# Optimization experiments

Measured on AMD Instinct MI355X. Metric: run time of the kernel, lower is better.

The kernel has to match this reference:

```python
import jax, jax.numpy as jnp
import numpy as np

EPS = 1e-12
H = 256
W = 256
RANK = 4
CTX = 1024
BATCH = 32
FF = (H + W) * RANK * 4  # 8192
STD = 0.001


def _norm(x, axis):
    # torch: (x - mean) / sqrt(var(unbiased) + eps)
    m = jnp.mean(x, axis=axis, keepdims=True)
    v = jnp.var(x, axis=axis, keepdims=True, ddof=1)
    return (x - m) / jnp.sqrt(v + EPS)


def _norm_polar(x):
    # x: [B, N, 2]; magnitude-normalize relative to per-batch max magnitude
    x_abs = jnp.sqrt(x[..., 0] ** 2 + x[..., 1] ** 2 + EPS)          # [B, N]
    h = x_abs / (jnp.max(x_abs, axis=-1, keepdims=True) + EPS)       # [B, N]
    xn = x / (x_abs[..., None] + EPS)                                # [B, N, 2]
    return jnp.stack([h * xn[..., 0], h * xn[..., 1]], axis=-1)


def setup_inputs() -> dict:
    key = jax.random.key(0)
    ks = jax.random.split(key, 12)

    def lin(k, fan_in, shape):
        b = 1.0 / np.sqrt(fan_in)
        return jax.random.uniform(k, shape, jnp.float32, -b, b)

    weights_static = jnp.concatenate([
        jax.random.normal(ks[9], (1, H, W, 2), jnp.float32) * STD,
        jax.random.normal(ks[10], (1, H, W, 2), jnp.float32) * STD
        + jnp.array([1.0, 0.0], jnp.float32),
    ], axis=0)  # [2, H, W, 2]

    return {
        "x": jax.random.normal(ks[0], (BATCH, CTX), jnp.float32),
        "W_in": lin(ks[1], CTX, (FF, CTX)),
        "b_in": lin(ks[2], CTX, (FF,)),
        "W_gate": lin(ks[3], CTX, (FF, CTX)),
        "b_gate": lin(ks[4], CTX, (FF,)),
        "W_t": lin(ks[5], FF, (FF, FF)),
        "b_t": lin(ks[6], FF, (FF,)),
        "conv_w": lin(ks[7], RANK, (RANK, RANK)),  # 1x1 conv kernel [out, in]
        "conv_b": lin(ks[8], RANK, (RANK,)),
        "weights_static": weights_static,
        "weights_mod": jax.random.normal(ks[11], (4, H, W), jnp.float32) * STD,
    }


def reference(x, W_in, b_in, W_gate, b_gate, W_t, b_t, conv_w, conv_b,
              weights_static, weights_mod):
    b = x.shape[0]
    # dual linear projections (dropout p=0 -> identity)
    xt = x @ W_in.T + b_in            # [B, FF]
    xg = x @ W_gate.T + b_gate        # [B, FF]
    stack = jnp.stack([xt, xg], axis=0).reshape(2, b, 4, -1)
    stack = _norm(stack, -1)
    ctx = (stack[0] * jnp.tanh(stack[1])).reshape(b, -1)   # gated, [B, FF]
    ctx = ctx @ W_t.T + b_t                                 # [B, FF]
    ctx = ctx.reshape(b, 4, RANK, H + W)
    modc = _norm(ctx, -1)
    # outer product -> [B, 4, RANK, H, W]
    mod = jnp.tanh(jnp.einsum('bkri,bkrj->bkrij', modc[..., :H], modc[..., H:]))
    # channel 0: 1x1 conv over rank channels, then sum channels (keepdim)
    mod_real = jnp.einsum('oi,bihw->bohw', conv_w, mod[:, 0]) + conv_b[None, :, None, None]
    mod_real = jnp.sum(mod_real, axis=1, keepdims=True)     # [B, 1, H, W]
    mod_other = jnp.sum(mod[:, 1:], axis=2)                 # [B, 3, H, W]
    mod = jnp.concatenate([mod_real, mod_other], axis=1)    # [B, 4, H, W]
    mod = weights_mod[None] * mod

    A0 = weights_static[0]            # [H, W, 2]
    A1 = weights_static[1]            # [H, W, 2]
    Bm = jnp.moveaxis(mod[:, 0:2], 1, -1)                   # [B, H, W, 2]
    ms_r = A1[..., 0] * Bm[..., 0] - A1[..., 1] * Bm[..., 1]
    ms_i = A1[..., 0] * Bm[..., 1] - A1[..., 1] * Bm[..., 0]
    mod_scaled = jnp.stack([ms_r, ms_i], axis=-1)           # [B, H, W, 2]
    mod_scaled = _norm_polar(mod_scaled.reshape(b, H * W, 2)).reshape(b, H, W, 2)

    mag = jnp.sqrt(mod_scaled[..., 0] ** 2 + mod_scaled[..., 1] ** 2 + EPS)
    mag = jnp.sqrt(jnp.mean(mag, axis=(-1, -2)) + EPS)      # [B]
    mod_scaled = mod_scaled / mag[:, None, None, None]

    mod_weights = A0[None] + mod_scaled                     # [B, H, W, 2]

    mod_proj = jnp.moveaxis(mod[:, 2:], 1, -1)              # [B, H, W, 2]
    mod_proj = _norm_polar(mod_proj.reshape(b, H * W, 2)).reshape(b, H, W, 2)
    den = jnp.sqrt(mod_proj[..., 0] ** 2 + mod_proj[..., 1] ** 2 + EPS)
    theta_cos = mod_proj[..., 0] / den
    theta_sin = mod_proj[..., 1] / den
    weights = mod_weights[..., 0] * theta_cos + mod_weights[..., 1] * theta_sin
    return weights  # [B, H, W]
```

## Files before the change

### kernel.cpp

```cpp
#include <hip/hip_runtime.h>
#include <cstddef>

#define NB   32
#define CTXD 1024
#define FFD  8192
#define HD   256
#define WD   256
#define NPIX 65536
#define EPSF 1e-12f
#define SCF  4096.0f
#define ISCF (1.0f/4096.0f)

typedef __attribute__((ext_vector_type(8))) _Float16 half8;
typedef __attribute__((ext_vector_type(4))) float f32x4;


__device__ __forceinline__ float ftanh(float x){
  float ax = fabsf(x);
  float e  = __expf(2.0f*ax);
  float r  = 1.0f - 2.0f*__builtin_amdgcn_rcpf(e + 1.0f);
  return copysignf(r, x);
}

__device__ __forceinline__ void split2h(float f, _Float16& h0, _Float16& h1){
  h0 = (_Float16)f;
  float r = (f - (float)h0) * SCF;
  h1 = (_Float16)r;
}

__device__ __forceinline__ void gload_lds16(const void* g, void* l){
  __builtin_amdgcn_global_load_lds(
      (__attribute__((address_space(1))) void*)g,
      (__attribute__((address_space(3))) void*)l, 16, 0, 0);
}

__device__ __forceinline__ void block_reduce4(float& a, float& b, float& c, float& d){
  for (int off = 32; off > 0; off >>= 1){
    a += __shfl_down(a, off); b += __shfl_down(b, off);
    c += __shfl_down(c, off); d += __shfl_down(d, off);
  }
  __shared__ float lds[16];
  int wid = threadIdx.x >> 6, lane = threadIdx.x & 63;
  if (lane == 0){ lds[wid*4+0]=a; lds[wid*4+1]=b; lds[wid*4+2]=c; lds[wid*4+3]=d; }
  __syncthreads();
  a = (lds[0]+lds[4])+(lds[8]+lds[12]);
  b = (lds[1]+lds[5])+(lds[9]+lds[13]);
  c = (lds[2]+lds[6])+(lds[10]+lds[14]);
  d = (lds[3]+lds[7])+(lds[11]+lds[15]);
}

__device__ __forceinline__ void pixel_core(
    const float* __restrict__ lds, int h, int w, int pix,
    float cw0, float cw1, float cw2, float cw3, float cb,
    const float* __restrict__ wmod, const float* __restrict__ wstat,
    float& r_, float& i_, float& p_, float& q_){
  float sk[4];
  #pragma unroll
  for (int k = 0; k < 4; ++k){
    float acc = 0.f;
    #pragma unroll
    for (int r = 0; r < 4; ++r){
      int kr = k*4 + r;
      float u  = lds[kr*512 + h];
      float vv = lds[kr*512 + 256 + w];
      float tt = ftanh(u*vv);
      float cwr = (r==0)?cw0:(r==1)?cw1:(r==2)?cw2:cw3;
      acc += (k==0) ? cwr*tt : tt;
    }
    sk[k] = acc;
  }
  sk[0] += cb;
  float m0 = sk[0]*wmod[0*NPIX+pix];
  float m1 = sk[1]*wmod[1*NPIX+pix];
  float m2 = sk[2]*wmod[2*NPIX+pix];
  float m3 = sk[3]*wmod[3*NPIX+pix];
  float2 A1 = *(const float2*)(wstat + (size_t)(NPIX + pix)*2);
  r_ = A1.x*m0 - A1.y*m1;
  i_ = A1.x*m1 - A1.y*m0;
  p_ = m2; q_ = m3;
}


__global__ __launch_bounds__(256) void k_prep(
    const float* __restrict__ x, unsigned short* __restrict__ P,
    float* __restrict__ red){
  int g = blockIdx.x*256 + threadIdx.x;
  if (g < 64) red[g] = 0.0f;
  int b = g >> 7, grp = g & 127;
  int c = grp >> 2, kg = grp & 3;
  const float* src = x + (size_t)b*CTXD + grp*8;
  float4 v0 = *(const float4*)(src), v1 = *(const float4*)(src+4);
  float vv[8] = {v0.x,v0.y,v0.z,v0.w,v1.x,v1.y,v1.z,v1.w};
  half8 g0, g1;
  #pragma unroll
  for (int e = 0; e < 8; ++e){
    _Float16 h0,h1; split2h(vv[e],h0,h1);
    g0[e]=h0; g1[e]=h1;
  }
  size_t base = (size_t)c*2048 + (b>>4)*512 + kg*128 + (b&15)*8;
  *(half8*)(P + base)        = g0;
  *(half8*)(P + base + 1024) = g1;
}

__global__ __launch_bounds__(256) void k_gemm_reuse(
    const float* __restrict__ W0, const float* __restrict__ W1,
    const unsigned short* __restrict__ BP,
    float* __restrict__ Cp, int K, size_t zstride){
  __shared__ float wtile[2][4096];
  __shared__ unsigned short bpack[16384];
  const int t = threadIdx.x;
  const int wv = t >> 6, lane = t & 63;
  const int row = lane & 15, kg = lane >> 4;
  const int f0 = blockIdx.x * 128;
  const int kc = blockIdx.y;
  const float* __restrict__ W = blockIdx.z ? W1 : W0;
  const int kb = kc * 256;

  {
    const unsigned short* bsrc = BP + (size_t)(kc*8)*2048;
    #pragma unroll
    for (int i = 0; i < 8; ++i){
      int call = wv*8 + i;
      gload_lds16(bsrc + call*512 + lane*8, bpack + call*512);
    }
  }
  auto stageW = [&](int buf, int s){
    const int kbase = kb + s*32;
    #pragma unroll
    for (int i = 0; i < 4; ++i){
      int call = wv*4 + i;
      const float* src = W + (size_t)(f0 + call*8 + (lane>>3))*K + kbase
                           + (((lane&7) ^ ((lane>>3)&7)) << 2);
      gload_lds16(src, &wtile[buf][call*256]);
    }
  };

  stageW(0, 0);
  asm volatile("s_waitcnt vmcnt(0)" ::: "memory");
  __syncthreads();

  f32x4 aH0l={0.f,0.f,0.f,0.f}, aH0h={0.f,0.f,0.f,0.f};
  f32x4 aL0l={0.f,0.f,0.f,0.f}, aL0h={0.f,0.f,0.f,0.f};
  f32x4 aH1l={0.f,0.f,0.f,0.f}, aH1h={0.f,0.f,0.f,0.f};
  f32x4 aL1l={0.f,0.f,0.f,0.f}, aL1h={0.f,0.f,0.f,0.f};
  int cur = 0;
  const int sw = row & 7;

  for (int s = 0; s < 8; ++s){
    if (s + 1 < 8) stageW(cur ^ 1, s + 1);
    asm volatile("s_waitcnt vmcnt(4)" ::: "memory");
    __builtin_amdgcn_sched_barrier(0);
    const unsigned short* bch = bpack + s*2048 + kg*128 + row*8;
    half8 b0l = *(const half8*)(bch);
    half8 b0h = *(const half8*)(bch +  512);
    half8 b1l = *(const half8*)(bch + 1024);
    half8 b1h = *(const half8*)(bch + 1536);
    #pragma unroll
    for (int T = 0; T < 2; ++T){
      const float* wr = &wtile[cur][(wv*32 + T*16 + row)*32];
      float4 lo = *(const float4*)(wr + (((2*kg  ) ^ sw) << 2));
      float4 hi = *(const float4*)(wr + (((2*kg+1) ^ sw) << 2));
      half8 a0, a1;
      float wv8[8] = {lo.x,lo.y,lo.z,lo.w,hi.x,hi.y,hi.z,hi.w};
      #pragma unroll
      for (int e = 0; e < 8; ++e){
        _Float16 h0,h1; split2h(wv8[e],h0,h1);
        a0[e]=h0; a1[e]=h1;
      }
      if (T == 0){
        aH0l = __builtin_amdgcn_mfma_f32_16x16x32_f16(a0, b0l, aH0l, 0,0,0);
        aH0h = __builtin_amdgcn_mfma_f32_16x16x32_f16(a0, b0h, aH0h, 0,0,0);
        aL0l = __builtin_amdgcn_mfma_f32_16x16x32_f16(a0, b1l, aL0l, 0,0,0);
        aL0h = __builtin_amdgcn_mfma_f32_16x16x32_f16(a0, b1h, aL0h, 0,0,0);
        aL0l = __builtin_amdgcn_mfma_f32_16x16x32_f16(a1, b0l, aL0l, 0,0,0);
        aL0h = __builtin_amdgcn_mfma_f32_16x16x32_f16(a1, b0h, aL0h, 0,0,0);
      } else {
        aH1l = __builtin_amdgcn_mfma_f32_16x16x32_f16(a0, b0l, aH1l, 0,0,0);
        aH1h = __builtin_amdgcn_mfma_f32_16x16x32_f16(a0, b0h, aH1h, 0,0,0);
        aL1l = __builtin_amdgcn_mfma_f32_16x16x32_f16(a0, b1l, aL1l, 0,0,0);
        aL1h = __builtin_amdgcn_mfma_f32_16x16x32_f16(a0, b1h, aL1h, 0,0,0);
        aL1l = __builtin_amdgcn_mfma_f32_16x16x32_f16(a1, b0l, aL1l, 0,0,0);
        aL1h = __builtin_amdgcn_mfma_f32_16x16x32_f16(a1, b0h, aL1h, 0,0,0);
      }
    }
    cur ^= 1;
  }

  float* __restrict__ C = Cp + (size_t)blockIdx.z*zstride + (size_t)kc*(FFD*32);
  #pragma unroll
  for (int r = 0; r < 4; ++r){
    int fA = f0 + wv*32 + kg*4 + r;
    int fB = fA + 16;
    C[(size_t)fA*32 + row]      = aH0l[r] + aL0l[r]*ISCF;
    C[(size_t)fA*32 + 16 + row] = aH0h[r] + aL0h[r]*ISCF;
    C[(size_t)fB*32 + row]      = aH1l[r] + aL1l[r]*ISCF;
    C[(size_t)fB*32 + 16 + row] = aH1h[r] + aL1h[r]*ISCF;
  }
}

__global__ __launch_bounds__(256) void k_reduce1(
    const float* __restrict__ Cp, const float* __restrict__ bin,
    const float* __restrict__ bg, float* __restrict__ xtT,
    float* __restrict__ xgT){
  int g = blockIdx.x*256 + threadIdx.x;
  int m = g >> 18, idx = g & 262143;
  int f = idx >> 5;
  const float* __restrict__ cp = Cp + (size_t)m*(4ull*FFD*32);
  float s = (m ? bg : bin)[f];
  #pragma unroll
  for (int sI = 0; sI < 4; ++sI) s += cp[(size_t)sI*(FFD*32) + idx];
  (m ? xgT : xtT)[idx] = s;
}

__global__ __launch_bounds__(256) void k_reduce2(
    const float* __restrict__ Cp, const float* __restrict__ bias,
    float* __restrict__ outT){
  int g = blockIdx.x*256 + threadIdx.x;
  int f = g >> 5;
  float s = bias[f];
  #pragma unroll
  for (int sI = 0; sI < 32; ++sI) s += Cp[(size_t)sI*(FFD*32) + g];
  outT[g] = s;
}

__global__ __launch_bounds__(256) void k_normgate(
    const float* __restrict__ xtT, const float* __restrict__ xgT,
    unsigned short* __restrict__ P){
  int b = blockIdx.x >> 2, g4 = blockIdx.x & 3;
  int t = threadIdx.x;
  int f8 = g4*2048 + t*8;
  float vt[8], vg[8];
  float st=0.f, sst=0.f, sg=0.f, ssg=0.f;
  #pragma unroll
  for (int i = 0; i < 8; ++i){
    int f = f8 + i;
    float a = xtT[(size_t)f*NB + b];
    float c = xgT[(size_t)f*NB + b];
    vt[i]=a; vg[i]=c;
    st += a; sst += a*a; sg += c; ssg += c*c;
  }
  block_reduce4(st, sst, sg, ssg);
  float mt = st * (1.0f/2048.0f);
  float it = rsqrtf((sst - st*mt) * (1.0f/2047.0f) + EPSF);
  float mg = sg * (1.0f/2048.0f);
  float ig = rsqrtf((ssg - sg*mg) * (1.0f/2047.0f) + EPSF);
  half8 g0, g1;
  #pragma unroll
  for (int i = 0; i < 8; ++i){
    float nt = (vt[i]-mt)*it;
    float ng = (vg[i]-mg)*ig;
    float cv = nt * ftanh(ng);
    _Float16 h0,h1; split2h(cv,h0,h1);
    g0[i]=h0; g1[i]=h1;
  }
  int c2 = f8 >> 5, kg = (f8 >> 3) & 3;
  size_t base = (size_t)c2*2048 + (b>>4)*512 + kg*128 + (b&15)*8;
  *(half8*)(P + base)        = g0;
  *(half8*)(P + base + 1024) = g1;
}

__global__ __launch_bounds__(256) void k_norm512(
    const float* __restrict__ ctx2T, float* __restrict__ modc){
  int b = blockIdx.x >> 4, kr = blockIdx.x & 15;
  int t = threadIdx.x;
  int base = kr*512;
  float v0 = ctx2T[(base + t      )*NB + b];
  float v1 = ctx2T[(base + 256 + t)*NB + b];
  float s = v0+v1, ss = v0*v0 + v1*v1, d0=0.f, d1=0.f;
  block_reduce4(s, ss, d0, d1);
  float m   = s * (1.0f/512.0f);
  float inv = rsqrtf((ss - s*m) * (1.0f/511.0f) + EPSF);
  modc[b*FFD + base + t      ] = (v0-m)*inv;
  modc[b*FFD + base + 256 + t] = (v1-m)*inv;
}

__global__ __launch_bounds__(256) void k_scan(
    const float* __restrict__ modc,
    const float* __restrict__ convw, const float* __restrict__ convb,
    const float* __restrict__ wmod, const float* __restrict__ wstat,
    float* __restrict__ red, float* __restrict__ magpart){
  int b = blockIdx.x >> 4, chunk = blockIdx.x & 15;
  int t = threadIdx.x;
  __shared__ float lds[16*512];
  #pragma unroll
  for (int i = 0; i < 8; ++i){
    float4 v = *(const float4*)(modc + (size_t)b*FFD + (i*256 + t)*4);
    *(float4*)(lds + (i*256 + t)*4) = v;
  }
  float cw0 = convw[0]+convw[4]+convw[8]+convw[12];
  float cw1 = convw[1]+convw[5]+convw[9]+convw[13];
  float cw2 = convw[2]+convw[6]+convw[10]+convw[14];
  float cw3 = convw[3]+convw[7]+convw[11]+convw[15];
  float cb  = convb[0]+convb[1]+convb[2]+convb[3];
  __syncthreads();
  int w = t;
  float mxs = 0.f, mxp = 0.f, sas = 0.f;
  for (int it = 0; it < 16; ++it){
    int h = chunk*16 + it;
    int pix = h*WD + w;
    float r_, i_, p_, q_;
    pixel_core(lds, h, w, pix, cw0, cw1, cw2, cw3, cb, wmod, wstat,
               r_, i_, p_, q_);
    float as = sqrtf(r_*r_ + i_*i_ + EPSF);
    float ap = sqrtf(p_*p_ + q_*q_ + EPSF);
    mxs = fmaxf(mxs, as); mxp = fmaxf(mxp, ap);
    sas += as;
  }
  for (int off = 32; off > 0; off >>= 1){
    mxs = fmaxf(mxs, __shfl_down(mxs, off));
    mxp = fmaxf(mxp, __shfl_down(mxp, off));
    sas += __shfl_down(sas, off);
  }
  __shared__ float lred[12];
  int wid = t >> 6, lane = t & 63;
  if (lane == 0){ lred[wid] = mxs; lred[4+wid] = mxp; lred[8+wid] = sas; }
  __syncthreads();
  if (t == 0){
    float a = fmaxf(fmaxf(lred[0],lred[1]), fmaxf(lred[2],lred[3]));
    float p = fmaxf(fmaxf(lred[4],lred[5]), fmaxf(lred[6],lred[7]));
    float s = (lred[8]+lred[9])+(lred[10]+lred[11]);
    atomicMax((int*)&red[b],    __float_as_int(a));
    atomicMax((int*)&red[32+b], __float_as_int(p));
    magpart[b*16 + chunk] = s;
  }
}

__global__ __launch_bounds__(256) void k_final(
    const float* __restrict__ modc,
    const float* __restrict__ convw, const float* __restrict__ convb,
    const float* __restrict__ wmod, const float* __restrict__ wstat,
    const float* __restrict__ red, const float* __restrict__ magpart,
    float* __restrict__ out){
  int b = blockIdx.x >> 4, chunk = blockIdx.x & 15;
  int t = threadIdx.x;
  __shared__ float lds[16*512];
  __shared__ float s_im;
  if (t < 16){
    float v = magpart[b*16 + t];
    for (int off = 8; off > 0; off >>= 1) v += __shfl_down(v, off);
    if (t == 0){
      float maxs = red[b];
      s_im = rsqrtf(v*(1.0f/65536.0f)/(maxs + EPSF) + EPSF);
    }
  }
  #pragma unroll
  for (int i = 0; i < 8; ++i){
    float4 v = *(const float4*)(modc + (size_t)b*FFD + (i*256 + t)*4);
    *(float4*)(lds + (i*256 + t)*4) = v;
  }
  float cw0 = convw[0]+convw[4]+convw[8]+convw[12];
  float cw1 = convw[1]+convw[5]+convw[9]+convw[13];
  float cw2 = convw[2]+convw[6]+convw[10]+convw[14];
  float cw3 = convw[3]+convw[7]+convw[11]+convw[15];
  float cb  = convb[0]+convb[1]+convb[2]+convb[3];
  __syncthreads();
  float im = s_im;
  float maxs = red[b], maxp = red[32+b];
  int w = t;
  for (int it = 0; it < 16; ++it){
    int h = chunk*16 + it;
    int pix = h*WD + w;
    float r_, i_, p_, q_;
    pixel_core(lds, h, w, pix, cw0, cw1, cw2, cw3, cb, wmod, wstat,
               r_, i_, p_, q_);
    float as = sqrtf(r_*r_ + i_*i_ + EPSF);
    float fs = (as/(maxs+EPSF))/(as+EPSF)*im;
    float2 A0 = *(const float2*)(wstat + (size_t)pix*2);
    float mwr = A0.x + fs*r_;
    float mwi = A0.y + fs*i_;
    float ap = sqrtf(p_*p_ + q_*q_ + EPSF);
    float fp = (ap/(maxp+EPSF))/(ap+EPSF);
    float mpr = fp*p_, mpi = fp*q_;
    float den = sqrtf(mpr*mpr + mpi*mpi + EPSF);
    out[(size_t)b*NPIX + pix] = (mwr*mpr + mwi*mpi)/den;
  }
}


extern "C" void kernel_launch(void* const* d_in, const int* in_sizes, int n_in,
                              void* d_out, int out_size, void* d_ws, size_t ws_size,
                              hipStream_t stream){
  const float* x     = (const float*)d_in[0];
  const float* Win   = (const float*)d_in[1];
  const float* bin   = (const float*)d_in[2];
  const float* Wg    = (const float*)d_in[3];
  const float* bg    = (const float*)d_in[4];
  const float* Wt    = (const float*)d_in[5];
  const float* bt    = (const float*)d_in[6];
  const float* convw = (const float*)d_in[7];
  const float* convb = (const float*)d_in[8];
  const float* wstat = (const float*)d_in[9];
  const float* wmod  = (const float*)d_in[10];
  float* out = (float*)d_out;
  float* ws  = (float*)d_ws;

  float* xtT   = ws;
  float* xgT   = ws + 262144;
  float* ctx2T = ws;
  float* modc  = ws + 262144;
  unsigned short* P2 = (unsigned short*)(ws + 524288);
  unsigned short* P1 = (unsigned short*)(ws + 917504);
  float* Cp    = ws + 966656;
  float* red     = ws + 9355264;
  float* magpart = ws + 9355328;

  k_prep<<<16, 256, 0, stream>>>(x, P1, red);
  k_gemm_reuse<<<dim3(64,4,2), 256, 0, stream>>>(Win, Wg, P1,
                                                 Cp, CTXD, 4ull*FFD*32);
  k_reduce1<<<2048, 256, 0, stream>>>(Cp, bin, bg, xtT, xgT);
  k_normgate<<<128, 256, 0, stream>>>(xtT, xgT, P2);
  k_gemm_reuse<<<dim3(64,32,1), 256, 0, stream>>>(Wt, Wt, P2,
                                                  Cp, FFD, 0);
  k_reduce2<<<1024, 256, 0, stream>>>(Cp, bt, ctx2T);
  k_norm512<<<512, 256, 0, stream>>>(ctx2T, modc);
  k_scan<<<512, 256, 0, stream>>>(modc, convw, convb, wmod, wstat, red, magpart);
  k_final<<<512, 256, 0, stream>>>(modc, convw, convb, wmod, wstat, red,
                                   magpart, out);
}
```

Before: 154.4 us.

## Fuse input packing into first GEMM and halve split-K count for second GEMM

```diff
diff --git a/kernel.cpp b/kernel.cpp
--- a/kernel.cpp
+++ b/kernel.cpp
@@ -81,31 +81,11 @@
 }
 
 
-__global__ __launch_bounds__(256) void k_prep(
-    const float* __restrict__ x, unsigned short* __restrict__ P,
-    float* __restrict__ red){
-  int g = blockIdx.x*256 + threadIdx.x;
-  if (g < 64) red[g] = 0.0f;
-  int b = g >> 7, grp = g & 127;
-  int c = grp >> 2, kg = grp & 3;
-  const float* src = x + (size_t)b*CTXD + grp*8;
-  float4 v0 = *(const float4*)(src), v1 = *(const float4*)(src+4);
-  float vv[8] = {v0.x,v0.y,v0.z,v0.w,v1.x,v1.y,v1.z,v1.w};
-  half8 g0, g1;
-  #pragma unroll
-  for (int e = 0; e < 8; ++e){
-    _Float16 h0,h1; split2h(vv[e],h0,h1);
-    g0[e]=h0; g1[e]=h1;
-  }
-  size_t base = (size_t)c*2048 + (b>>4)*512 + kg*128 + (b&15)*8;
-  *(half8*)(P + base)        = g0;
-  *(half8*)(P + base + 1024) = g1;
-}
-
-__global__ __launch_bounds__(256) void k_gemm_reuse(
+template<int STEPS, bool PACKB>
+__global__ __launch_bounds__(256) void k_gemm(
     const float* __restrict__ W0, const float* __restrict__ W1,
-    const unsigned short* __restrict__ BP,
-    float* __restrict__ Cp, int K, size_t zstride){
+    const unsigned short* __restrict__ BP, const float* __restrict__ X,
+    float* __restrict__ Cp, float* __restrict__ red, int K, size_t zstride){
   __shared__ float wtile[2][4096];
   __shared__ unsigned short bpack[16384];
   const int t = threadIdx.x;
@@ -114,10 +94,30 @@
   const int f0 = blockIdx.x * 128;
   const int kc = blockIdx.y;
   const float* __restrict__ W = blockIdx.z ? W1 : W0;
-  const int kb = kc * 256;
-
-  {
-    const unsigned short* bsrc = BP + (size_t)(kc*8)*2048;
+  const int kb = kc * (STEPS*32);
+
+  if (PACKB && blockIdx.x == 0 && blockIdx.y == 0 && blockIdx.z == 0 && t < 64)
+    red[t] = 0.0f;
+
+  if constexpr (PACKB){
+    for (int u = t; u < 1024; u += 256){
+      int b = u >> 5, grp = u & 31;
+      const float* src = X + (size_t)b*K + kb + grp*8;
+      float4 v0 = *(const float4*)(src), v1 = *(const float4*)(src+4);
+      float vv[8] = {v0.x,v0.y,v0.z,v0.w,v1.x,v1.y,v1.z,v1.w};
+      half8 g0, g1;
+      #pragma unroll
+      for (int e = 0; e < 8; ++e){
+        _Float16 h0,h1; split2h(vv[e],h0,h1);
+        g0[e]=h0; g1[e]=h1;
+      }
+      int c = grp >> 2, kgp = grp & 3;
+      size_t base = (size_t)c*2048 + (b>>4)*512 + kgp*128 + (b&15)*8;
+      *(half8*)(bpack + base)        = g0;
+      *(half8*)(bpack + base + 1024) = g1;
+    }
+  } else {
+    const unsigned short* bsrc = BP + (size_t)(kc*STEPS)*2048;
     #pragma unroll
     for (int i = 0; i < 8; ++i){
       int call = wv*8 + i;
@@ -146,11 +146,22 @@
   int cur = 0;
   const int sw = row & 7;
 
-  for (int s = 0; s < 8; ++s){
-    if (s + 1 < 8) stageW(cur ^ 1, s + 1);
+  for (int s = 0; s < STEPS; ++s){
+    if constexpr (STEPS > 8){
+      if (s == 8){
+        __syncthreads();
+        const unsigned short* bsrc = BP + (size_t)(kc*STEPS + 8)*2048;
+        #pragma unroll
+        for (int i = 0; i < 8; ++i){
+          int call = wv*8 + i;
+          gload_lds16(bsrc + call*512 + lane*8, bpack + call*512);
+        }
+      }
+    }
+    if (s + 1 < STEPS) stageW(cur ^ 1, s + 1);
     asm volatile("s_waitcnt vmcnt(4)" ::: "memory");
     __builtin_amdgcn_sched_barrier(0);
-    const unsigned short* bch = bpack + s*2048 + kg*128 + row*8;
+    const unsigned short* bch = bpack + (size_t)(s & 7)*2048 + kg*128 + row*8;
     half8 b0l = *(const half8*)(bch);
     half8 b0h = *(const half8*)(bch +  512);
     half8 b1l = *(const half8*)(bch + 1024);
@@ -219,7 +230,7 @@
   int f = g >> 5;
   float s = bias[f];
   #pragma unroll
-  for (int sI = 0; sI < 32; ++sI) s += Cp[(size_t)sI*(FFD*32) + g];
+  for (int sI = 0; sI < 16; ++sI) s += Cp[(size_t)sI*(FFD*32) + g];
   outT[g] = s;
 }
 
@@ -399,18 +410,16 @@
   float* ctx2T = ws;
   float* modc  = ws + 262144;
   unsigned short* P2 = (unsigned short*)(ws + 524288);
-  unsigned short* P1 = (unsigned short*)(ws + 917504);
   float* Cp    = ws + 966656;
   float* red     = ws + 9355264;
   float* magpart = ws + 9355328;
 
-  k_prep<<<16, 256, 0, stream>>>(x, P1, red);
-  k_gemm_reuse<<<dim3(64,4,2), 256, 0, stream>>>(Win, Wg, P1,
-                                                 Cp, CTXD, 4ull*FFD*32);
+  k_gemm<8,true><<<dim3(64,4,2), 256, 0, stream>>>(Win, Wg, nullptr, x,
+                                                   Cp, red, CTXD, 4ull*FFD*32);
   k_reduce1<<<2048, 256, 0, stream>>>(Cp, bin, bg, xtT, xgT);
   k_normgate<<<128, 256, 0, stream>>>(xtT, xgT, P2);
-  k_gemm_reuse<<<dim3(64,32,1), 256, 0, stream>>>(Wt, Wt, P2,
-                                                  Cp, FFD, 0);
+  k_gemm<16,false><<<dim3(64,16,1), 256, 0, stream>>>(Wt, Wt, P2, nullptr,
+                                                      Cp, red, FFD, 0);
   k_reduce2<<<1024, 256, 0, stream>>>(Cp, bt, ctx2T);
   k_norm512<<<512, 256, 0, stream>>>(ctx2T, modc);
   k_scan<<<512, 256, 0, stream>>>(modc, convw, convb, wmod, wstat, red, magpart);
```

After: 152.2 us. Within noise of the previous version (-1.4%).
